# Optimization experiments

Measured on AMD Instinct MI355X. Metric: run time of the kernel, lower is better.

## Reference

```python
import jax, jax.numpy as jnp
import numpy as np

B, D, H, S = 32768, 512, 8, 3  # batch, stream_dim, heads, num_streams
DH = D // H
EPS = 1e-5


def setup_inputs() -> dict:
    key = jax.random.key(0)
    ks = jax.random.split(key, 16)
    sc = lambda fan_in: 1.0 / np.sqrt(fan_in)
    return {
        "kinematic_h": jax.random.normal(ks[0], (B, D), jnp.float32),
        "color_h": jax.random.normal(ks[1], (B, D), jnp.float32),
        "spinor_h": jax.random.normal(ks[2], (B, D), jnp.float32),
        # MultiheadAttention packed in-proj and out-proj
        "w_in": jax.random.normal(ks[3], (3 * D, D), jnp.float32) * sc(D),
        "b_in": jnp.zeros((3 * D,), jnp.float32),
        "w_out": jax.random.normal(ks[4], (D, D), jnp.float32) * sc(D),
        "b_out": jnp.zeros((D,), jnp.float32),
        # stream gate: Linear(3D -> 3) + softmax
        "w_gate": jax.random.normal(ks[5], (S, S * D), jnp.float32) * sc(S * D),
        "b_gate": jnp.zeros((S,), jnp.float32),
        # fusion MLP: Linear(3D -> 2D), SiLU, Linear(2D -> D)
        "w1": jax.random.normal(ks[6], (2 * D, S * D), jnp.float32) * sc(S * D),
        "b1": jnp.zeros((2 * D,), jnp.float32),
        "w2": jax.random.normal(ks[7], (D, 2 * D), jnp.float32) * sc(2 * D),
        "b2": jnp.zeros((D,), jnp.float32),
        # LayerNorm
        "gamma": jnp.ones((D,), jnp.float32),
        "beta": jnp.zeros((D,), jnp.float32),
    }


def reference(kinematic_h, color_h, spinor_h, w_in, b_in, w_out, b_out,
              w_gate, b_gate, w1, b1, w2, b2, gamma, beta):
    stacked = jnp.stack([kinematic_h, color_h, spinor_h], axis=1)  # [B,S,D]
    b = stacked.shape[0]
    # self-attention (Q=K=V=stacked), packed QKV projection
    qkv = stacked @ w_in.T + b_in  # [B,S,3D]
    q, k, v = jnp.split(qkv, 3, axis=-1)
    q = q.reshape(b, S, H, DH)
    k = k.reshape(b, S, H, DH)
    v = v.reshape(b, S, H, DH)
    scores = jnp.einsum("bqhd,bkhd->bhqk", q, k) / np.sqrt(DH)
    attn = jax.nn.softmax(scores, axis=-1)
    out = jnp.einsum("bhqk,bkhd->bqhd", attn, v).reshape(b, S, D)
    attn_out = stacked + (out @ w_out.T + b_out)  # residual, [B,S,D]
    # gating softmax over streams
    flat = attn_out.reshape(b, S * D)
    gates = jax.nn.softmax(flat @ w_gate.T + b_gate, axis=-1)[..., None]  # [B,S,1]
    gated = (attn_out * gates).reshape(b, S * D)
    # fusion MLP (dropout=eval no-op)
    h = jax.nn.silu(gated @ w1.T + b1)
    fused = h @ w2.T + b2  # [B,D]
    # LayerNorm
    mu = jnp.mean(fused, axis=-1, keepdims=True)
    var = jnp.var(fused, axis=-1, keepdims=True)
    return (fused - mu) * jax.lax.rsqrt(var + EPS) * gamma + beta
```

## Files before the change

kernel.cpp:

```cpp
#include <hip/hip_runtime.h>
#include <hip/hip_bf16.h>
#include <stdint.h>


typedef float f32x4 __attribute__((ext_vector_type(4)));
typedef short bf16x8 __attribute__((ext_vector_type(8)));

__device__ __forceinline__ float bf2f(unsigned short h) {
  return __uint_as_float(((unsigned)h) << 16);
}
__device__ __forceinline__ unsigned short f2bf(float f) {
  __hip_bfloat16 h = __float2bfloat16(f);
  return *reinterpret_cast<unsigned short*>(&h);
}
__device__ __forceinline__ unsigned pack2bf(float lo, float hi) {
  __hip_bfloat162 h2 = __float22bfloat162_rn(make_float2(lo, hi));
  return *reinterpret_cast<unsigned*>(&h2);
}
__device__ __forceinline__ uint2 f2bf4p(float4 v) {
  return make_uint2(pack2bf(v.x, v.y), pack2bf(v.z, v.w));
}

__device__ __forceinline__ void async_cp16(const void* g, void* lds) {
  __builtin_amdgcn_global_load_lds(
      (const __attribute__((address_space(1))) void*)g,
      (__attribute__((address_space(3))) void*)lds, 16, 0, 0);
}

__global__ void __launch_bounds__(256) cvtall(const float4* __restrict__ w_in,
                                              const float4* __restrict__ w_out,
                                              const float4* __restrict__ w1,
                                              const float4* __restrict__ w2,
                                              uint2* __restrict__ dst) {
  int i = blockIdx.x * 256 + threadIdx.x;
  const float4* s;
  int off;
  if (i < 196608)      { s = w_in;  off = 0; }
  else if (i < 262144) { s = w_out; off = 196608; }
  else if (i < 655360) { s = w1;    off = 262144; }
  else                 { s = w2;    off = 655360; }
  dst[i] = f2bf4p(s[i - off]);
}

__global__ void __launch_bounds__(256)
qkv_attn(const float* __restrict__ X0,
         const float* __restrict__ X1,
         const float* __restrict__ X2,
         const unsigned short* __restrict__ Wi,
         const float* __restrict__ bin,
         unsigned short* __restrict__ Sout,
         unsigned short* __restrict__ AO) {
  __shared__ unsigned short lds[96 * 200];
  unsigned short* Abuf = lds;
  unsigned short* Bbuf = lds + 6144;

  const int t = threadIdx.x;
  const int lane = t & 63;
  const int wave = t >> 6;
  const int wm = wave >> 1, wn = wave & 1;

  const int ny = gridDim.y;
  const int id = blockIdx.y * 8 + blockIdx.x;
  const int xcd = id & 7, j = id >> 3;
  const int h = j & 7;
  const long m0 = (long)(xcd * (ny >> 3) + (j >> 3)) * 96;

  const int trow = t >> 3;
  const int swz = ((t & 7) ^ (trow & 7)) << 3;
  const long b0 = m0 / 3;
  const float* Aptr[3];
  unsigned short* Sptr[3];
#pragma unroll
  for (int r = 0; r < 3; r++) {
    const int rl = trow + 32 * r;
    const int br = rl / 3;
    const int sr = rl - 3 * br;
    const float* X = (sr == 0) ? X0 : (sr == 1) ? X1 : X2;
    Aptr[r] = X + (b0 + br) * 512 + swz;
    Sptr[r] = Sout + (m0 + rl) * 512 + swz;
  }
  const unsigned short* Bg = Wi + ((long)h * 64 + trow) * 512 + swz;
  unsigned short* AsD = Abuf + t * 8;
  unsigned short* BsD = Bbuf + t * 8;

  f32x4 acc[3][6] = {};
  const int arow0 = wm * 48 + (lane & 15);
  const int brow0 = wn * 96 + (lane & 15);

  float4 Alo[3], Ahi[3];
#pragma unroll
  for (int r = 0; r < 3; r++) {
    Alo[r] = *(const float4*)(Aptr[r]);
    Ahi[r] = *(const float4*)(Aptr[r] + 4);
  }

  for (int k0 = 0; k0 < 512; k0 += 64) {
    __syncthreads();
    const bool sw = ((k0 >> 6) == h);
#pragma unroll
    for (int r = 0; r < 3; r++) {
      const uint4 uv = make_uint4(
          pack2bf(Alo[r].x, Alo[r].y), pack2bf(Alo[r].z, Alo[r].w),
          pack2bf(Ahi[r].x, Ahi[r].y), pack2bf(Ahi[r].z, Ahi[r].w));
      *(uint4*)(AsD + r * 2048) = uv;
      if (sw) *(uint4*)(Sptr[r] + k0) = uv;
    }
#pragma unroll
    for (int r = 0; r < 6; r++)
      async_cp16(Bg + (long)((r >> 1) * 512 + (r & 1) * 32) * 512 + k0, BsD + r * 2048);
    __syncthreads();
    if (k0 + 64 < 512) {
#pragma unroll
      for (int r = 0; r < 3; r++) {
        Alo[r] = *(const float4*)(Aptr[r] + k0 + 64);
        Ahi[r] = *(const float4*)(Aptr[r] + k0 + 68);
      }
    }
#pragma unroll
    for (int kk = 0; kk < 2; kk++) {
      const int sc = ((kk * 4 + (lane >> 4)) ^ (lane & 7)) << 3;
      bf16x8 af[3], bfr[6];
#pragma unroll
      for (int mt = 0; mt < 3; mt++)
        af[mt] = *(const bf16x8*)&Abuf[(arow0 + mt * 16) * 64 + sc];
#pragma unroll
      for (int nt = 0; nt < 6; nt++)
        bfr[nt] = *(const bf16x8*)&Bbuf[(brow0 + nt * 16) * 64 + sc];
#pragma unroll
      for (int mt = 0; mt < 3; mt++)
#pragma unroll
        for (int nt = 0; nt < 6; nt++)
          acc[mt][nt] = __builtin_amdgcn_mfma_f32_16x16x32_bf16(
              af[mt], bfr[nt], acc[mt][nt], 0, 0, 0);
    }
  }

  __syncthreads();
  const int crow0 = wm * 48 + ((lane >> 4) << 2);
  const int ccol0 = wn * 96 + (lane & 15);
#pragma unroll
  for (int nt = 0; nt < 6; nt++) {
    const int col = ccol0 + nt * 16;
    const float bv = bin[(col >> 6) * 512 + h * 64 + (col & 63)];
#pragma unroll
    for (int mt = 0; mt < 3; mt++) {
      const int rb = (crow0 + mt * 16) * 200 + col;
      const unsigned p01 = pack2bf(acc[mt][nt][0] + bv, acc[mt][nt][1] + bv);
      const unsigned p23 = pack2bf(acc[mt][nt][2] + bv, acc[mt][nt][3] + bv);
      lds[rb]       = (unsigned short)p01;
      lds[rb + 200] = (unsigned short)(p01 >> 16);
      lds[rb + 400] = (unsigned short)p23;
      lds[rb + 600] = (unsigned short)(p23 >> 16);
    }
  }
  __syncthreads();

  const int bi = lane >> 3;
  const int l8 = lane & 7;
  const int r0 = (wave * 8 + bi) * 3;
  float q[3][8], k[3][8], v[3][8];
#pragma unroll
  for (int s = 0; s < 3; s++) {
    const unsigned short* rowp = &lds[(r0 + s) * 200 + l8 * 8];
    uint4 qu = *(const uint4*)(rowp);
    uint4 ku = *(const uint4*)(rowp + 64);
    uint4 vu = *(const uint4*)(rowp + 128);
    const unsigned* qw = (const unsigned*)&qu;
    const unsigned* kw = (const unsigned*)&ku;
    const unsigned* vw = (const unsigned*)&vu;
#pragma unroll
    for (int jj = 0; jj < 4; jj++) {
      q[s][2 * jj]     = __uint_as_float(qw[jj] << 16);
      q[s][2 * jj + 1] = __uint_as_float(qw[jj] & 0xffff0000u);
      k[s][2 * jj]     = __uint_as_float(kw[jj] << 16);
      k[s][2 * jj + 1] = __uint_as_float(kw[jj] & 0xffff0000u);
      v[s][2 * jj]     = __uint_as_float(vw[jj] << 16);
      v[s][2 * jj + 1] = __uint_as_float(vw[jj] & 0xffff0000u);
    }
  }
  float p[3][3];
#pragma unroll
  for (int s = 0; s < 3; s++)
#pragma unroll
    for (int u = 0; u < 3; u++) {
      float d = 0.f;
#pragma unroll
      for (int e = 0; e < 8; e++) d = fmaf(q[s][e], k[u][e], d);
      p[s][u] = d;
    }
#pragma unroll
  for (int m = 1; m < 8; m <<= 1)
#pragma unroll
    for (int s = 0; s < 3; s++)
#pragma unroll
      for (int u = 0; u < 3; u++) p[s][u] += __shfl_xor(p[s][u], m, 64);

  unsigned short* ob = AO + (m0 + r0) * 512 + h * 64 + l8 * 8;
#pragma unroll
  for (int s = 0; s < 3; s++) {
    float a0 = p[s][0] * 0.125f, a1 = p[s][1] * 0.125f, a2 = p[s][2] * 0.125f;
    float mx = fmaxf(a0, fmaxf(a1, a2));
    float e0 = __expf(a0 - mx), e1 = __expf(a1 - mx), e2 = __expf(a2 - mx);
    float inv = 1.0f / (e0 + e1 + e2);
    unsigned ow[4];
#pragma unroll
    for (int jj = 0; jj < 4; jj++) {
      float lo = (e0 * v[0][2 * jj] + e1 * v[1][2 * jj] + e2 * v[2][2 * jj]) * inv;
      float hi = (e0 * v[0][2 * jj + 1] + e1 * v[1][2 * jj + 1] + e2 * v[2][2 * jj + 1]) * inv;
      ow[jj] = pack2bf(lo, hi);
    }
    *(uint4*)(ob + s * 512) = *(uint4*)ow;
  }
}

enum { EPI_BF16 = 0, EPI_RES = 1, EPI_SILU = 2, EPI_F32 = 3 };

template <int EPI>
__global__ void __launch_bounds__(256)
gemm_bt(const unsigned short* __restrict__ A,
        const unsigned short* __restrict__ W,
        const float* __restrict__ bias,
        const unsigned short* __restrict__ Res,
        void* __restrict__ Out,
        int K, int N) {
  __shared__ unsigned short As[128 * 64];
  __shared__ unsigned short Bs[128 * 64];
  const int t = threadIdx.x;
  const int lane = t & 63;
  const int wave = t >> 6;
  const int wm = wave >> 1, wn = wave & 1;

  const int nb = gridDim.x;
  const int nblocks = nb * gridDim.y;
  const int id = blockIdx.y * nb + blockIdx.x;
  const int lid = ((nblocks & 7) == 0) ? ((id & 7) * (nblocks >> 3) + (id >> 3)) : id;
  const long bm = (long)(lid / nb) * 128;
  const long bn = (long)(lid % nb) * 128;

  const int srow = t >> 3;
  const int schunk = ((t & 7) ^ (srow & 7)) << 3;
  const unsigned short* Ag = A + (bm + srow) * (long)K + schunk;
  const unsigned short* Wg = W + (bn + srow) * (long)K + schunk;
  unsigned short* AsD = As + t * 8;
  unsigned short* BsD = Bs + t * 8;

  f32x4 acc[4][4] = {};
  const int arow0 = wm * 64 + (lane & 15);
  const int brow0 = wn * 64 + (lane & 15);

  for (int k0 = 0; k0 < K; k0 += 64) {
    __syncthreads();
#pragma unroll
    for (int i = 0; i < 4; i++) {
      async_cp16(Ag + (long)(i * 32) * K + k0, AsD + i * 2048);
      async_cp16(Wg + (long)(i * 32) * K + k0, BsD + i * 2048);
    }
    __syncthreads();
#pragma unroll
    for (int kk = 0; kk < 2; kk++) {
      const int sc = ((kk * 4 + (lane >> 4)) ^ (lane & 7)) << 3;
      bf16x8 af[4], bfr[4];
#pragma unroll
      for (int mt = 0; mt < 4; mt++)
        af[mt] = *(const bf16x8*)&As[(arow0 + mt * 16) * 64 + sc];
#pragma unroll
      for (int nt = 0; nt < 4; nt++)
        bfr[nt] = *(const bf16x8*)&Bs[(brow0 + nt * 16) * 64 + sc];
#pragma unroll
      for (int mt = 0; mt < 4; mt++)
#pragma unroll
        for (int nt = 0; nt < 4; nt++)
          acc[mt][nt] = __builtin_amdgcn_mfma_f32_16x16x32_bf16(
              af[mt], bfr[nt], acc[mt][nt], 0, 0, 0);
    }
  }

  const long row0 = bm + wm * 64 + ((lane >> 4) << 2);
  const int col0 = (int)bn + wn * 64 + (lane & 15);
#pragma unroll
  for (int nt = 0; nt < 4; nt++) {
    const int col = col0 + nt * 16;
    const float bv = bias[col];
#pragma unroll
    for (int mt = 0; mt < 4; mt++) {
      const long rbase = row0 + mt * 16;
#pragma unroll
      for (int r = 0; r < 4; r++) {
        float v = acc[mt][nt][r] + bv;
        const long idx = (rbase + r) * (long)N + col;
        if (EPI == EPI_RES) v += bf2f(Res[idx]);
        if (EPI == EPI_SILU) v = v * (1.0f / (1.0f + __expf(-v)));
        if (EPI == EPI_F32)
          ((float*)Out)[idx] = v;
        else
          ((unsigned short*)Out)[idx] = f2bf(v);
      }
    }
  }
}

__global__ void __launch_bounds__(512)
gemm_ln(const unsigned short* __restrict__ A,
        const unsigned short* __restrict__ W,
        const float* __restrict__ bias,
        const float* __restrict__ gamma,
        const float* __restrict__ beta,
        float* __restrict__ Out,
        int K) {
  __shared__ unsigned short As[64 * 64];
  __shared__ unsigned short Bs[512 * 64];
  __shared__ float stats[8][64][2];
  const int t = threadIdx.x;
  const int lane = t & 63;
  const int wave = t >> 6;

  const int nblocks = gridDim.x;
  const int id = blockIdx.x;
  const int lid = ((nblocks & 7) == 0) ? ((id & 7) * (nblocks >> 3) + (id >> 3)) : id;
  const long bm = (long)lid * 64;

  const int srow = t >> 3;
  const int sch = ((t & 7) ^ (srow & 7)) << 3;
  const unsigned short* Ag = A + (bm + srow) * (long)K + sch;
  const unsigned short* Wg = W + (long)srow * K + sch;
  unsigned short* AsD = As + t * 8;
  unsigned short* BsD = Bs + t * 8;

  f32x4 acc[4][4] = {};
  const int arow0 = lane & 15;
  const int brow0 = wave * 64 + (lane & 15);

  for (int k0 = 0; k0 < K; k0 += 64) {
    __syncthreads();
    async_cp16(Ag + k0, AsD);
#pragma unroll
    for (int i = 0; i < 8; i++)
      async_cp16(Wg + (long)(i * 64) * K + k0, BsD + i * 4096);
    __syncthreads();
#pragma unroll
    for (int kk = 0; kk < 2; kk++) {
      const int sc = ((kk * 4 + (lane >> 4)) ^ (lane & 7)) << 3;
      bf16x8 af[4], bfr[4];
#pragma unroll
      for (int mt = 0; mt < 4; mt++)
        af[mt] = *(const bf16x8*)&As[(arow0 + mt * 16) * 64 + sc];
#pragma unroll
      for (int nt = 0; nt < 4; nt++)
        bfr[nt] = *(const bf16x8*)&Bs[(brow0 + nt * 16) * 64 + sc];
#pragma unroll
      for (int mt = 0; mt < 4; mt++)
#pragma unroll
        for (int nt = 0; nt < 4; nt++)
          acc[mt][nt] = __builtin_amdgcn_mfma_f32_16x16x32_bf16(
              af[mt], bfr[nt], acc[mt][nt], 0, 0, 0);
    }
  }

  const int colb = wave * 64 + (lane & 15);
  float bv[4], gm[4], be[4];
#pragma unroll
  for (int nt = 0; nt < 4; nt++) {
    bv[nt] = bias[colb + nt * 16];
    gm[nt] = gamma[colb + nt * 16];
    be[nt] = beta[colb + nt * 16];
  }
#pragma unroll
  for (int mt = 0; mt < 4; mt++)
#pragma unroll
    for (int r = 0; r < 4; r++) {
      float s = 0.f, ss = 0.f;
#pragma unroll
      for (int nt = 0; nt < 4; nt++) {
        const float v = acc[mt][nt][r] + bv[nt];
        s += v; ss += v * v;
      }
#pragma unroll
      for (int m = 1; m < 16; m <<= 1) {
        s += __shfl_xor(s, m, 64);
        ss += __shfl_xor(ss, m, 64);
      }
      if ((lane & 15) == 0) {
        const int rl = mt * 16 + ((lane >> 4) << 2) + r;
        stats[wave][rl][0] = s;
        stats[wave][rl][1] = ss;
      }
    }
  __syncthreads();
#pragma unroll
  for (int mt = 0; mt < 4; mt++)
#pragma unroll
    for (int r = 0; r < 4; r++) {
      const int rl = mt * 16 + ((lane >> 4) << 2) + r;
      float s = 0.f, ss = 0.f;
#pragma unroll
      for (int w = 0; w < 8; w++) {
        s += stats[w][rl][0];
        ss += stats[w][rl][1];
      }
      const float mean = s * (1.0f / 512.0f);
      const float var = ss * (1.0f / 512.0f) - mean * mean;
      const float rstd = rsqrtf(var + 1e-5f);
      float* orow = Out + (bm + rl) * 512;
#pragma unroll
      for (int nt = 0; nt < 4; nt++) {
        const float v = acc[mt][nt][r] + bv[nt];
        orow[colb + nt * 16] = (v - mean) * rstd * gm[nt] + be[nt];
      }
    }
}

__global__ void __launch_bounds__(256) gate3(const unsigned short* AT,
                                             const float* __restrict__ WG,
                                             const float* __restrict__ BG,
                                             unsigned short* G) {
  int row = blockIdx.x * 4 + (threadIdx.x >> 6);
  int lane = threadIdx.x & 63;
  const unsigned short* rp = AT + (long)row * 1536 + lane * 8;
  float x[3][8];
  float p[3] = {0.f, 0.f, 0.f};
#pragma unroll
  for (int seg = 0; seg < 3; seg++) {
    uint4 u = *(const uint4*)(rp + seg * 512);
    const unsigned* uw = (const unsigned*)&u;
#pragma unroll
    for (int j = 0; j < 4; j++) {
      x[seg][2 * j]     = __uint_as_float(uw[j] << 16);
      x[seg][2 * j + 1] = __uint_as_float(uw[j] & 0xffff0000u);
    }
    const int e0 = seg * 512 + lane * 8;
#pragma unroll
    for (int g = 0; g < 3; g++) {
      const float* wp = WG + g * 1536 + e0;
#pragma unroll
      for (int e = 0; e < 8; e++) p[g] = fmaf(x[seg][e], wp[e], p[g]);
    }
  }
#pragma unroll
  for (int m = 1; m < 64; m <<= 1)
#pragma unroll
    for (int g = 0; g < 3; g++) p[g] += __shfl_xor(p[g], m, 64);
  float g0 = p[0] + BG[0], g1 = p[1] + BG[1], g2 = p[2] + BG[2];
  float mx = fmaxf(g0, fmaxf(g1, g2));
  g0 = __expf(g0 - mx); g1 = __expf(g1 - mx); g2 = __expf(g2 - mx);
  float inv = 1.0f / (g0 + g1 + g2);
  float gs[3] = {g0 * inv, g1 * inv, g2 * inv};
  unsigned short* op = G + (long)row * 1536 + lane * 8;
#pragma unroll
  for (int seg = 0; seg < 3; seg++) {
    unsigned ow[4];
#pragma unroll
    for (int j = 0; j < 4; j++)
      ow[j] = pack2bf(x[seg][2 * j] * gs[seg], x[seg][2 * j + 1] * gs[seg]);
    *(uint4*)(op + seg * 512) = *(uint4*)ow;
  }
}

extern "C" void kernel_launch(void* const* d_in, const int* in_sizes, int n_in,
                              void* d_out, int out_size, void* d_ws, size_t ws_size,
                              hipStream_t stream) {
  const float* kin    = (const float*)d_in[0];
  const float* colr   = (const float*)d_in[1];
  const float* spi    = (const float*)d_in[2];
  const float* w_in   = (const float*)d_in[3];
  const float* b_in   = (const float*)d_in[4];
  const float* w_out  = (const float*)d_in[5];
  const float* b_out  = (const float*)d_in[6];
  const float* w_gate = (const float*)d_in[7];
  const float* b_gate = (const float*)d_in[8];
  const float* w1     = (const float*)d_in[9];
  const float* b1     = (const float*)d_in[10];
  const float* w2     = (const float*)d_in[11];
  const float* b2     = (const float*)d_in[12];
  const float* gamma  = (const float*)d_in[13];
  const float* beta   = (const float*)d_in[14];
  float* out = (float*)d_out;

  long Bc = 32768;
  while (Bc > 1024 && (size_t)(6291456 + 9216 * Bc) > ws_size) Bc >>= 1;
  const int nch = (int)(32768 / Bc);

  char* ws = (char*)d_ws;
  unsigned short* Wic = (unsigned short*)(ws);
  unsigned short* Woc = (unsigned short*)(ws + 1572864);
  unsigned short* W1c = (unsigned short*)(ws + 2097152);
  unsigned short* W2c = (unsigned short*)(ws + 5242880);
  char* Sb  = ws + 6291456;
  char* AOb = Sb + 3072 * Bc;
  char* ATb = AOb + 3072 * Bc;

  cvtall<<<3072, 256, 0, stream>>>((const float4*)w_in, (const float4*)w_out,
                                   (const float4*)w1, (const float4*)w2,
                                   (uint2*)ws);

  for (int c = 0; c < nch; c++) {
    const long boff = (long)c * Bc;
    unsigned short* S_c  = (unsigned short*)Sb;
    unsigned short* AO_c = (unsigned short*)AOb;
    unsigned short* AT_c = (unsigned short*)ATb;
    unsigned short* G_c  = AT_c;
    unsigned short* H_c  = (unsigned short*)AOb;

    qkv_attn<<<dim3(8, (int)(Bc / 32)), 256, 0, stream>>>(
        kin + boff * 512, colr + boff * 512, spi + boff * 512,
        Wic, b_in, S_c, AO_c);
    gemm_bt<EPI_RES><<<dim3(4, (int)(3 * Bc / 128)), 256, 0, stream>>>(
        AO_c, Woc, b_out, S_c, AT_c, 512, 512);
    gate3<<<(int)(Bc / 4), 256, 0, stream>>>(AT_c, w_gate, b_gate, G_c);
    gemm_bt<EPI_SILU><<<dim3(8, (int)(Bc / 128)), 256, 0, stream>>>(
        G_c, W1c, b1, nullptr, H_c, 1536, 1024);
    gemm_ln<<<(int)(Bc / 64), 512, 0, stream>>>(
        H_c, W2c, b2, gamma, beta, out + boff * 512, 1024);
  }
}
```

Baseline: 782.8 us.

## Add 256x256-tile pipelined SiLU GEMM kernel for fusion MLP first layer

Replaces the generic 128-tile gemm_bt SiLU launch with a dedicated 512-thread kernel that computes 256x256 output tiles. It double-buffers LDS using async global-to-LDS loads interleaved between MFMA phases, uses an XOR-swizzled LDS layout, raises wave priority around MFMA blocks, and remaps block IDs for better L2 locality. The intent is higher arithmetic intensity and better overlap of loads with compute on the largest GEMM. The cost is heavy LDS use (128KB) and register pressure from 32 accumulator tiles, which limits occupancy to one block per CU.

```diff
diff --git a/kernel.cpp b/kernel.cpp
--- a/kernel.cpp
+++ b/kernel.cpp
@@ -294,6 +294,152 @@
           ((float*)Out)[idx] = v;
         else
           ((unsigned short*)Out)[idx] = f2bf(v);
+      }
+    }
+  }
+}
+
+__global__ void __launch_bounds__(512)
+gemm_silu256(const unsigned short* __restrict__ A,
+             const unsigned short* __restrict__ W,
+             const float* __restrict__ bias,
+             unsigned short* __restrict__ Out) {
+  constexpr int K = 1536, N = 1024, NT = 24;
+  constexpr int NSH = 8192, NDB = 16384;
+  __shared__ unsigned short As[2 * NDB];
+  __shared__ unsigned short Bs[2 * NDB];
+  const int t = threadIdx.x;
+  const int lane = t & 63;
+  const int wave = t >> 6;
+  const int wm = wave >> 2, wn = wave & 3;
+  const int l15 = lane & 15, lg = lane >> 4;
+
+  const int nb = gridDim.x;
+  const int nblocks = nb * gridDim.y;
+  const int id = blockIdx.y * nb + blockIdx.x;
+  const int lid = (id & 7) * (nblocks >> 3) + (id >> 3);
+  const long bm = (long)(lid / nb) * 256;
+  const long bn = (long)(lid % nb) * 256;
+
+  const int r0s = t >> 2, pc = t & 3;
+  const int c0 = pc ^ ((r0s >> 1) & 3);
+  const int r1s = r0s + 128;
+  const int c1 = pc ^ ((r1s >> 1) & 3);
+  const unsigned short* Ag0 = A + (bm + r0s) * (long)K + c0 * 8;
+  const unsigned short* Ag1 = A + (bm + r1s) * (long)K + c1 * 8;
+  const unsigned short* Wg0 = W + (bn + r0s) * (long)K + c0 * 8;
+  const unsigned short* Wg1 = W + (bn + r1s) * (long)K + c1 * 8;
+
+#define STA(d, kh, kb) do { \
+    async_cp16(Ag0 + (kb), &As[(d) * NDB + (kh) * NSH + t * 8]); \
+    async_cp16(Ag1 + (kb), &As[(d) * NDB + (kh) * NSH + 4096 + t * 8]); } while (0)
+#define STB(d, kh, kb) do { \
+    async_cp16(Wg0 + (kb), &Bs[(d) * NDB + (kh) * NSH + t * 8]); \
+    async_cp16(Wg1 + (kb), &Bs[(d) * NDB + (kh) * NSH + 4096 + t * 8]); } while (0)
+
+  const int ach = (lg ^ ((l15 >> 1) & 3)) << 3;
+  const int aoff = (wm * 128 + l15) * 32 + ach;
+  const int boff = (wn * 64 + l15) * 32 + ach;
+
+  f32x4 acc[8][4] = {};
+
+  STA(0, 0, 0);  STB(0, 0, 0);
+  STA(0, 1, 32); STB(0, 1, 32);
+  STA(1, 0, 64); STB(1, 0, 64);
+  asm volatile("s_waitcnt vmcnt(8)" ::: "memory");
+  __builtin_amdgcn_s_barrier();
+
+  for (int tt = 0; tt < NT; ++tt) {
+    const int d = tt & 1, dn = d ^ 1;
+    const bool s1 = (tt + 1 < NT), s2 = (tt + 2 < NT);
+    const int kb1 = (tt + 1) * 64, kb2 = (tt + 2) * 64;
+    const unsigned short* Ab = &As[d * NDB];
+    const unsigned short* Bb = &Bs[d * NDB];
+    bf16x8 af[4], bfr[4];
+
+#pragma unroll
+    for (int i = 0; i < 4; ++i) af[i] = *(const bf16x8*)&Ab[aoff + i * 512];
+#pragma unroll
+    for (int i = 0; i < 4; ++i) bfr[i] = *(const bf16x8*)&Bb[boff + i * 512];
+    if (s1) STA(dn, 1, kb1 + 32);
+    __builtin_amdgcn_s_barrier();
+    asm volatile("s_waitcnt lgkmcnt(0)" ::: "memory");
+    __builtin_amdgcn_s_setprio(1);
+#pragma unroll
+    for (int mi = 0; mi < 4; ++mi)
+#pragma unroll
+      for (int ni = 0; ni < 4; ++ni)
+        acc[mi][ni] = __builtin_amdgcn_mfma_f32_16x16x32_bf16(
+            af[mi], bfr[ni], acc[mi][ni], 0, 0, 0);
+    __builtin_amdgcn_s_setprio(0);
+    __builtin_amdgcn_s_barrier();
+
+#pragma unroll
+    for (int i = 0; i < 4; ++i) af[i] = *(const bf16x8*)&Ab[aoff + (4 + i) * 512];
+    if (s1) STB(dn, 1, kb1 + 32);
+    __builtin_amdgcn_s_barrier();
+    asm volatile("s_waitcnt lgkmcnt(0)" ::: "memory");
+    __builtin_amdgcn_s_setprio(1);
+#pragma unroll
+    for (int mi = 0; mi < 4; ++mi)
+#pragma unroll
+      for (int ni = 0; ni < 4; ++ni)
+        acc[4 + mi][ni] = __builtin_amdgcn_mfma_f32_16x16x32_bf16(
+            af[mi], bfr[ni], acc[4 + mi][ni], 0, 0, 0);
+    __builtin_amdgcn_s_setprio(0);
+    asm volatile("s_waitcnt vmcnt(8)" ::: "memory");
+    __builtin_amdgcn_s_barrier();
+
+#pragma unroll
+    for (int i = 0; i < 4; ++i) af[i] = *(const bf16x8*)&Ab[NSH + aoff + i * 512];
+#pragma unroll
+    for (int i = 0; i < 4; ++i) bfr[i] = *(const bf16x8*)&Bb[NSH + boff + i * 512];
+    if (s2) STA(d, 0, kb2);
+    __builtin_amdgcn_s_barrier();
+    asm volatile("s_waitcnt lgkmcnt(0)" ::: "memory");
+    __builtin_amdgcn_s_setprio(1);
+#pragma unroll
+    for (int mi = 0; mi < 4; ++mi)
+#pragma unroll
+      for (int ni = 0; ni < 4; ++ni)
+        acc[mi][ni] = __builtin_amdgcn_mfma_f32_16x16x32_bf16(
+            af[mi], bfr[ni], acc[mi][ni], 0, 0, 0);
+    __builtin_amdgcn_s_setprio(0);
+    __builtin_amdgcn_s_barrier();
+
+#pragma unroll
+    for (int i = 0; i < 4; ++i) af[i] = *(const bf16x8*)&Ab[NSH + aoff + (4 + i) * 512];
+    if (s2) STB(d, 0, kb2);
+    __builtin_amdgcn_s_barrier();
+    asm volatile("s_waitcnt lgkmcnt(0)" ::: "memory");
+    __builtin_amdgcn_s_setprio(1);
+#pragma unroll
+    for (int mi = 0; mi < 4; ++mi)
+#pragma unroll
+      for (int ni = 0; ni < 4; ++ni)
+        acc[4 + mi][ni] = __builtin_amdgcn_mfma_f32_16x16x32_bf16(
+            af[mi], bfr[ni], acc[4 + mi][ni], 0, 0, 0);
+    __builtin_amdgcn_s_setprio(0);
+    asm volatile("s_waitcnt vmcnt(8)" ::: "memory");
+    __builtin_amdgcn_s_barrier();
+  }
+#undef STA
+#undef STB
+
+  const long grow0 = bm + wm * 128 + (lg << 2);
+  const int col0 = (int)bn + wn * 64 + l15;
+#pragma unroll
+  for (int nt = 0; nt < 4; ++nt) {
+    const int col = col0 + nt * 16;
+    const float bv = bias[col];
+#pragma unroll
+    for (int mt = 0; mt < 8; ++mt) {
+      const long rb = grow0 + mt * 16;
+#pragma unroll
+      for (int r = 0; r < 4; ++r) {
+        float v = acc[mt][nt][r] + bv;
+        v = v * (1.0f / (1.0f + __expf(-v)));
+        Out[(rb + r) * (long)N + col] = f2bf(v);
       }
     }
   }
@@ -506,8 +652,8 @@
     gemm_bt<EPI_RES><<<dim3(4, (int)(3 * Bc / 128)), 256, 0, stream>>>(
         AO_c, Woc, b_out, S_c, AT_c, 512, 512);
     gate3<<<(int)(Bc / 4), 256, 0, stream>>>(AT_c, w_gate, b_gate, G_c);
-    gemm_bt<EPI_SILU><<<dim3(8, (int)(Bc / 128)), 256, 0, stream>>>(
-        G_c, W1c, b1, nullptr, H_c, 1536, 1024);
+    gemm_silu256<<<dim3(4, (int)(Bc / 256)), 512, 0, stream>>>(
+        G_c, W1c, b1, H_c);
     gemm_ln<<<(int)(Bc / 64), 512, 0, stream>>>(
         H_c, W2c, b2, gamma, beta, out + boff * 512, 1024);
   }
```

Result: faster. 746.1 us (-4.7%).
